# Performance work log

Measured on AMD Instinct MI355X. Metric: run time of the kernel, lower is better.

## Reference

```python
import jax, jax.numpy as jnp
import numpy as np

N = 50000; E = 800000
GNN_IN = 256; MLP_IN = 256; HID = 512; F_DIM = 128; H = 2; NCLS = 40
HC = H * F_DIM  # 256


def setup_inputs() -> dict:
    key = jax.random.key(0)
    ks = jax.random.split(key, 24)
    w = lambda k, shape: (jax.random.normal(k, shape, jnp.float32) * 0.05)
    inp = {
        'x_gsage': jax.random.normal(ks[0], (N, GNN_IN), jnp.float32),
        'edge_index': jax.random.randint(ks[1], (2, E), 0, N),
        'x_mlp': jax.random.normal(ks[2], (N, MLP_IN), jnp.float32),
        # TransformerConv params (query/key/value/skip linears)
        'Wq': w(ks[3], (HC, GNN_IN)), 'bq': jnp.zeros(HC, jnp.float32),
        'Wk': w(ks[4], (HC, GNN_IN)), 'bk': jnp.zeros(HC, jnp.float32),
        'Wv': w(ks[5], (HC, GNN_IN)), 'bv': jnp.zeros(HC, jnp.float32),
        'Wskip': w(ks[6], (HC, GNN_IN)), 'bskip': jnp.zeros(HC, jnp.float32),
        # MLP (num_layers=3): in->hid, hid->hid, hid->2*F_DIM; 2 batchnorms
        'W1': w(ks[7], (HID, MLP_IN)), 'b1': jnp.zeros(HID, jnp.float32),
        'g1': jnp.ones(HID, jnp.float32), 'be1': jnp.zeros(HID, jnp.float32),
        'W2': w(ks[8], (HID, HID)), 'b2': jnp.zeros(HID, jnp.float32),
        'g2': jnp.ones(HID, jnp.float32), 'be2': jnp.zeros(HID, jnp.float32),
        'W3': w(ks[9], (HC, HID)), 'b3': jnp.zeros(HC, jnp.float32),
        # fusion scalars
        'alpha': jnp.array([0.5], jnp.float32), 'beta': jnp.array([0.5], jnp.float32),
        # classifier head
        'Wc1': w(ks[10], (HID, HC)), 'bc1': jnp.zeros(HID, jnp.float32),
        'Wc2': w(ks[11], (NCLS, HID)), 'bc2': jnp.zeros(NCLS, jnp.float32),
    }
    return inp


def _lin(x, W, b):
    return x @ W.T + b


def _batchnorm(x, g, b, eps=1e-5):
    mu = jnp.mean(x, axis=0)
    var = jnp.var(x, axis=0)
    return (x - mu) * jax.lax.rsqrt(var + eps) * g + b


def _transformer_conv(x, edge_index, Wq, bq, Wk, bk, Wv, bv, Wskip, bskip):
    # PyG TransformerConv, heads=H, concat=True, root_weight=True (eval: no dropout)
    q = _lin(x, Wq, bq).reshape(N, H, F_DIM)
    k = _lin(x, Wk, bk).reshape(N, H, F_DIM)
    v = _lin(x, Wv, bv).reshape(N, H, F_DIM)
    src, dst = edge_index[0], edge_index[1]
    # per-edge, per-head attention logits  [E, H]
    logits = jnp.einsum('ehd,ehd->eh', q[dst], k[src]) / jnp.sqrt(jnp.float32(F_DIM))
    # segment softmax over incoming edges of each destination node
    amax = jax.ops.segment_max(logits, dst, num_segments=N)  # [N, H]
    amax = jnp.where(jnp.isfinite(amax), amax, 0.0)
    ex = jnp.exp(logits - amax[dst])                           # [E, H]
    denom = jax.ops.segment_sum(ex, dst, num_segments=N)      # [N, H]
    attn = ex / jnp.maximum(denom[dst], 1e-16)                 # [E, H]
    msg = v[src] * attn[:, :, None]                            # [E, H, C]
    out = jax.ops.segment_sum(msg, dst, num_segments=N)       # [N, H, C]
    out = out.reshape(N, HC) + _lin(x, Wskip, bskip)
    return out


def reference(x_gsage, edge_index, x_mlp, Wq, bq, Wk, bk, Wv, bv, Wskip, bskip,
              W1, b1, g1, be1, W2, b2, g2, be2, W3, b3, alpha, beta,
              Wc1, bc1, Wc2, bc2):
    h_g = _transformer_conv(x_gsage, edge_index, Wq, bq, Wk, bk, Wv, bv, Wskip, bskip)
    # MLP branch: (lin -> BN(batch stats) -> sigmoid) x2, then final lin; dropout off (eval)
    h = jax.nn.sigmoid(_batchnorm(_lin(x_mlp, W1, b1), g1, be1))
    h = jax.nn.sigmoid(_batchnorm(_lin(h, W2, b2), g2, be2))
    h_m = _lin(h, W3, b3)
    h_fused = alpha * h_g + beta * h_m
    out = _lin(jax.nn.relu(_lin(h_fused, Wc1, bc1)), Wc2, bc2)
    return out
```

## Files before the change

### kernel.cpp

```cpp
#include <hip/hip_runtime.h>
#include <hip/hip_bf16.h>
#include <cstdint>
#include <cstddef>

typedef __attribute__((ext_vector_type(8))) short short8;
typedef __attribute__((ext_vector_type(4))) float f32x4;

__device__ inline ushort f2bs(float f) {
    __hip_bfloat16 h = __float2bfloat16(f);
    return *(ushort*)&h;
}
__device__ inline float bu2f(ushort u) {
    return __uint_as_float(((unsigned)u) << 16);
}

template <int AB, int BM, int KT, int SIG>
__global__ __launch_bounds__(256) void gemm_fullk(
    const void* __restrict__ Avoid, const short* __restrict__ Wb,
    const float* __restrict__ bias, ushort* __restrict__ C,
    const float* __restrict__ scale, const float* __restrict__ shift,
    int M, int NT, int act)
{
    constexpr int KQ = KT / 32;
    __shared__ short As[BM][KT + 8];
    __shared__ short Bs[128][40];

    const int tid = threadIdx.x;
    const int lane = tid & 63;
    const int w = tid >> 6;
    const int wm = w >> 1, wn = w & 1;
    constexpr int MI = BM / 32;
    const int m0 = blockIdx.x * BM;
    const int lr = lane & 15;
    const int lk = (lane >> 4) * 8;
    const int Ntot = NT * 128;

    {
        constexpr int TPR = KT / 128;
        const int arow = tid / TPR;
        const int ac0 = (tid % TPR) * 128;
        const bool ok = (m0 + arow) < M;
        if (AB == 0) {
            const float* ap = (const float*)Avoid + (size_t)(m0 + arow) * KT + ac0;
#pragma unroll
            for (int j = 0; j < 16; ++j) {
                float4 x = ok ? *(const float4*)(ap + j * 8)
                              : make_float4(0.f, 0.f, 0.f, 0.f);
                float4 y = ok ? *(const float4*)(ap + j * 8 + 4)
                              : make_float4(0.f, 0.f, 0.f, 0.f);
                short8 v;
                v[0] = f2bs(x.x); v[1] = f2bs(x.y); v[2] = f2bs(x.z); v[3] = f2bs(x.w);
                v[4] = f2bs(y.x); v[5] = f2bs(y.y); v[6] = f2bs(y.z); v[7] = f2bs(y.w);
                *(short8*)&As[arow][ac0 + j * 8] = v;
            }
        } else {
            const short* ap = (const short*)Avoid + (size_t)(m0 + arow) * KT + ac0;
#pragma unroll
            for (int j = 0; j < 16; ++j) {
                short8 v = {};
                if (ok) v = *(const short8*)(ap + j * 8);
                if (SIG) {
#pragma unroll
                    for (int e = 0; e < 8; ++e) {
                        int c = ac0 + j * 8 + e;
                        float f = bu2f((ushort)v[e]) * scale[c] + shift[c];
                        v[e] = (short)f2bs(1.f / (1.f + __expf(-f)));
                    }
                }
                *(short8*)&As[arow][ac0 + j * 8] = v;
            }
        }
    }

    const int trow = tid >> 1;
    const int tcg = (tid & 1) * 16;

    short8 r0, r1;
    {
        const short* wp = Wb + (size_t)trow * KT + tcg;
        r0 = *(const short8*)wp;
        r1 = *(const short8*)(wp + 8);
    }

    f32x4 acc[MI][4] = {};
    const int total = NT * KQ;

    for (int idx = 0; idx < total; ++idx) {
        *(short8*)&Bs[trow][tcg] = r0;
        *(short8*)&Bs[trow][tcg + 8] = r1;
        __syncthreads();

        const int nidx = idx + 1;
        if (nidx < total) {
            const int nt = nidx / KQ, nk = (nidx % KQ) * 32;
            const short* wp = Wb + (size_t)(nt * 128 + trow) * KT + nk + tcg;
            r0 = *(const short8*)wp;
            r1 = *(const short8*)(wp + 8);
        }

        const int k0 = (idx % KQ) * 32;
        short8 afr[MI], bfr[4];
#pragma unroll
        for (int mi = 0; mi < MI; ++mi)
            afr[mi] = *(const short8*)&As[wm * (BM / 2) + mi * 16 + lr][k0 + lk];
#pragma unroll
        for (int nj = 0; nj < 4; ++nj)
            bfr[nj] = *(const short8*)&Bs[wn * 64 + nj * 16 + lr][lk];
#pragma unroll
        for (int mi = 0; mi < MI; ++mi)
#pragma unroll
            for (int nj = 0; nj < 4; ++nj)
                acc[mi][nj] = __builtin_amdgcn_mfma_f32_16x16x32_bf16(
                    afr[mi], bfr[nj], acc[mi][nj], 0, 0, 0);
        __syncthreads();

        if ((idx % KQ) == KQ - 1) {
            const int t = idx / KQ;
#pragma unroll
            for (int mi = 0; mi < MI; ++mi) {
#pragma unroll
                for (int nj = 0; nj < 4; ++nj) {
                    int gn = t * 128 + wn * 64 + nj * 16 + lr;
                    float b = bias[gn];
#pragma unroll
                    for (int r = 0; r < 4; ++r) {
                        int gm = m0 + wm * (BM / 2) + mi * 16 + (lane >> 4) * 4 + r;
                        if (gm < M) {
                            float v = acc[mi][nj][r] + b;
                            if (act == 1) v = fmaxf(v, 0.f);
                            C[(size_t)gm * Ntot + gn] = f2bs(v);
                        }
                    }
                    acc[mi][nj] = (f32x4){0.f, 0.f, 0.f, 0.f};
                }
            }
        }
    }
}

__global__ __launch_bounds__(256) void mfma_gemm_small(
    const short* __restrict__ A, const float* __restrict__ W,
    const float* __restrict__ bias, float* __restrict__ Cf,
    int M, int K, int Nout)
{
    __shared__ short As[128][40];
    __shared__ short Bs[128][40];
    const int tid = threadIdx.x;
    const int lane = tid & 63;
    const int w = tid >> 6;
    const int wm = w >> 1, wn = w & 1;
    const int m0 = blockIdx.y * 128, n0 = blockIdx.x * 128;
    const int trow = tid >> 1;
    const int tcg = (tid & 1) * 16;
    const int lr = lane & 15;
    const int lk = (lane >> 4) * 8;

    f32x4 acc[4][4] = {};

    for (int k0 = 0; k0 < K; k0 += 32) {
        {
            bool ok = (m0 + trow) < M;
            const short* ap = A + (size_t)(m0 + trow) * K + k0 + tcg;
            short8 s0 = {}, s1 = {};
            if (ok) { s0 = *(const short8*)(ap); s1 = *(const short8*)(ap + 8); }
            *(short8*)&As[trow][tcg] = s0;
            *(short8*)&As[trow][tcg + 8] = s1;
        }
        {
            short v[16];
            bool ok = (n0 + trow) < Nout;
            const float* wp = W + (size_t)(n0 + trow) * K + k0 + tcg;
#pragma unroll
            for (int q = 0; q < 4; ++q) {
                float4 t4 = ok ? *(const float4*)(wp + q * 4)
                               : make_float4(0.f, 0.f, 0.f, 0.f);
                v[q * 4 + 0] = f2bs(t4.x); v[q * 4 + 1] = f2bs(t4.y);
                v[q * 4 + 2] = f2bs(t4.z); v[q * 4 + 3] = f2bs(t4.w);
            }
            short8 w0, w1;
#pragma unroll
            for (int j = 0; j < 8; ++j) { w0[j] = v[j]; w1[j] = v[j + 8]; }
            *(short8*)&Bs[trow][tcg] = w0;
            *(short8*)&Bs[trow][tcg + 8] = w1;
        }
        __syncthreads();
        short8 afr[4], bfr[4];
#pragma unroll
        for (int mi = 0; mi < 4; ++mi)
            afr[mi] = *(const short8*)&As[wm * 64 + mi * 16 + lr][lk];
#pragma unroll
        for (int nj = 0; nj < 4; ++nj)
            bfr[nj] = *(const short8*)&Bs[wn * 64 + nj * 16 + lr][lk];
#pragma unroll
        for (int mi = 0; mi < 4; ++mi)
#pragma unroll
            for (int nj = 0; nj < 4; ++nj)
                acc[mi][nj] = __builtin_amdgcn_mfma_f32_16x16x32_bf16(
                    afr[mi], bfr[nj], acc[mi][nj], 0, 0, 0);
        __syncthreads();
    }
#pragma unroll
    for (int mi = 0; mi < 4; ++mi)
#pragma unroll
        for (int nj = 0; nj < 4; ++nj) {
            int gn = n0 + wn * 64 + nj * 16 + lr;
            if (gn >= Nout) continue;
            float b = bias[gn];
#pragma unroll
            for (int r = 0; r < 4; ++r) {
                int gm = m0 + wm * 64 + mi * 16 + (lane >> 4) * 4 + r;
                if (gm < M) Cf[(size_t)gm * Nout + gn] = acc[mi][nj][r] + b;
            }
        }
}

__global__ void zero_words(unsigned* __restrict__ p, size_t n)
{
    size_t i = (size_t)blockIdx.x * blockDim.x + threadIdx.x;
    size_t stride = (size_t)gridDim.x * blockDim.x;
    for (; i < n; i += stride) p[i] = 0u;
}

__global__ void pack_params(
    const float* __restrict__ Wq, const float* __restrict__ Wk,
    const float* __restrict__ Wv, const float* __restrict__ Wskip,
    const float* __restrict__ W1, const float* __restrict__ W2,
    const float* __restrict__ W3, const float* __restrict__ Wc1,
    const float* __restrict__ bq, const float* __restrict__ bk,
    const float* __restrict__ bv, const float* __restrict__ bskip,
    ushort* __restrict__ Wall, float* __restrict__ bcat)
{
    int q = blockIdx.x * 256 + threadIdx.x;
    if (q < 229376) {
        const float* s; int base4;
        if      (q < 16384)  { s = Wq;    base4 = 0; }
        else if (q < 32768)  { s = Wk;    base4 = 16384; }
        else if (q < 49152)  { s = Wv;    base4 = 32768; }
        else if (q < 65536)  { s = Wskip; base4 = 49152; }
        else if (q < 98304)  { s = W1;    base4 = 65536; }
        else if (q < 163840) { s = W2;    base4 = 98304; }
        else if (q < 196608) { s = W3;    base4 = 163840; }
        else                 { s = Wc1;   base4 = 196608; }
        float4 v = ((const float4*)s)[q - base4];
        ushort4 o;
        o.x = f2bs(v.x); o.y = f2bs(v.y); o.z = f2bs(v.z); o.w = f2bs(v.w);
        ((ushort4*)Wall)[q] = o;
    } else if (q < 229632) {
        int j = q - 229376;
        const float* s = (j < 64) ? bq : (j < 128) ? bk : (j < 192) ? bv : bskip;
        ((float4*)bcat)[j] = ((const float4*)s)[j & 63];
    }
}

__global__ __launch_bounds__(256) void bn_stats512_b(
    const ushort* __restrict__ X, float* __restrict__ sums,
    float* __restrict__ sumsq, int M)
{
    int t = threadIdx.x;
    float s0 = 0.f, q0 = 0.f, s1 = 0.f, q1 = 0.f;
    for (int r = blockIdx.x; r < M; r += gridDim.x) {
        ushort2 v = *(const ushort2*)(X + (size_t)r * 512 + 2 * t);
        float a = bu2f(v.x), b = bu2f(v.y);
        s0 += a; q0 += a * a;
        s1 += b; q1 += b * b;
    }
    atomicAdd(&sums[2 * t], s0);
    atomicAdd(&sumsq[2 * t], q0);
    atomicAdd(&sums[2 * t + 1], s1);
    atomicAdd(&sumsq[2 * t + 1], q1);
}

__global__ void bn_finalize(const float* __restrict__ sums,
                            const float* __restrict__ sumsq,
                            const float* __restrict__ g,
                            const float* __restrict__ be,
                            float* __restrict__ scale, float* __restrict__ shift,
                            int M, int C)
{
    int c = blockIdx.x * blockDim.x + threadIdx.x;
    if (c >= C) return;
    float mean = sums[c] / (float)M;
    float var = sumsq[c] / (float)M - mean * mean;
    float inv = rsqrtf(var + 1e-5f);
    float sc = g[c] * inv;
    scale[c] = sc;
    shift[c] = be[c] - mean * sc;
}

__global__ void count_edges(const int* __restrict__ ei, int* __restrict__ counts, int E)
{
    int i = blockIdx.x * 256 + threadIdx.x;
    if (i < E) atomicAdd(&counts[ei[E + i]], 1);
}

__global__ __launch_bounds__(256) void scan_local(
    const int* __restrict__ cnt, int* __restrict__ excl,
    int* __restrict__ bsums, int n)
{
    __shared__ int s[256];
    int t = threadIdx.x;
    int i = blockIdx.x * 256 + t;
    int v = (i < n) ? cnt[i] : 0;
    s[t] = v;
    __syncthreads();
    for (int off = 1; off < 256; off <<= 1) {
        int u = (t >= off) ? s[t - off] : 0;
        __syncthreads();
        s[t] += u;
        __syncthreads();
    }
    if (i < n) excl[i] = s[t] - v;
    if (t == 255) bsums[blockIdx.x] = s[255];
}

__global__ __launch_bounds__(256) void scan_top(int* __restrict__ bsums, int nb)
{
    __shared__ int s[256];
    int t = threadIdx.x;
    int v = (t < nb) ? bsums[t] : 0;
    s[t] = v;
    __syncthreads();
    for (int off = 1; off < 256; off <<= 1) {
        int u = (t >= off) ? s[t - off] : 0;
        __syncthreads();
        s[t] += u;
        __syncthreads();
    }
    if (t < nb) bsums[t] = s[t] - v;
}

__global__ void scan_add(int* __restrict__ excl, const int* __restrict__ bsums,
                         int* __restrict__ cursor, int n)
{
    int i = blockIdx.x * 256 + threadIdx.x;
    if (i < n) {
        int v = excl[i] + bsums[blockIdx.x];
        excl[i] = v;
        cursor[i] = v;
    }
}

__global__ void fill_edges(const int* __restrict__ ei, int* __restrict__ cursor,
                           int* __restrict__ esrc, int E)
{
    int i = blockIdx.x * 256 + threadIdx.x;
    if (i < E) {
        int dst = ei[E + i];
        int pos = atomicAdd(&cursor[dst], 1);
        esrc[pos] = ei[i];
    }
}

__global__ __launch_bounds__(256) void edge_attn(
    const int* __restrict__ esrc, const int* __restrict__ offs,
    const int* __restrict__ cnts, const ushort* __restrict__ QKVS,
    const ushort* __restrict__ hmb, const float* __restrict__ alpha,
    const float* __restrict__ beta, ushort* __restrict__ hf, int N)
{
    int node = blockIdx.x * 4 + (threadIdx.x >> 6);
    int lane = threadIdx.x & 63;
    if (node >= N) return;
    int start = offs[node];
    int cnt = cnts[node];

    ushort4 qu = *(const ushort4*)(QKVS + (size_t)node * 1024 + lane * 4);
    float qx = bu2f(qu.x), qy = bu2f(qu.y), qz = bu2f(qu.z), qw = bu2f(qu.w);
    const float s = 0.088388347648318447f;

    float m = -INFINITY, d = 0.f;
    float a0 = 0.f, a1 = 0.f, a2 = 0.f, a3 = 0.f;

    ushort4 ku_n = {}, vu_n = {};
    if (cnt > 0) {
        int src0 = esrc[start];
        ku_n = *(const ushort4*)(QKVS + (size_t)src0 * 1024 + 256 + lane * 4);
        vu_n = *(const ushort4*)(QKVS + (size_t)src0 * 1024 + 512 + lane * 4);
    }
    for (int i = 0; i < cnt; ++i) {
        ushort4 ku = ku_n, vu = vu_n;
        if (i + 1 < cnt) {
            int srcn = esrc[start + i + 1];
            ku_n = *(const ushort4*)(QKVS + (size_t)srcn * 1024 + 256 + lane * 4);
            vu_n = *(const ushort4*)(QKVS + (size_t)srcn * 1024 + 512 + lane * 4);
        }
        float p = qx * bu2f(ku.x) + qy * bu2f(ku.y)
                + qz * bu2f(ku.z) + qw * bu2f(ku.w);
        p += __shfl_xor(p, 1);
        p += __shfl_xor(p, 2);
        p += __shfl_xor(p, 4);
        p += __shfl_xor(p, 8);
        p += __shfl_xor(p, 16);
        float l = p * s;
        float mn = fmaxf(m, l);
        float sc = __expf(m - mn);
        float pe = __expf(l - mn);
        d = d * sc + pe;
        a0 = a0 * sc + pe * bu2f(vu.x);
        a1 = a1 * sc + pe * bu2f(vu.y);
        a2 = a2 * sc + pe * bu2f(vu.z);
        a3 = a3 * sc + pe * bu2f(vu.w);
        m = mn;
    }
    float invd = (cnt > 0) ? 1.f / fmaxf(d, 1e-16f) : 0.f;
    float o0 = a0 * invd, o1 = a1 * invd, o2 = a2 * invd, o3 = a3 * invd;

    ushort4 su = *(const ushort4*)(QKVS + (size_t)node * 1024 + 768 + lane * 4);
    ushort4 hm = *(const ushort4*)(hmb + (size_t)node * 256 + lane * 4);
    float al = alpha[0], be = beta[0];
    ushort4 o;
    o.x = f2bs(al * (o0 + bu2f(su.x)) + be * bu2f(hm.x));
    o.y = f2bs(al * (o1 + bu2f(su.y)) + be * bu2f(hm.y));
    o.z = f2bs(al * (o2 + bu2f(su.z)) + be * bu2f(hm.z));
    o.w = f2bs(al * (o3 + bu2f(su.w)) + be * bu2f(hm.w));
    *(ushort4*)(hf + (size_t)node * 256 + lane * 4) = o;
}

extern "C" void kernel_launch(void* const* d_in, const int* in_sizes, int n_in,
                              void* d_out, int out_size, void* d_ws, size_t ws_size,
                              hipStream_t stream)
{
    const float* x_g   = (const float*)d_in[0];
    const int*   ei    = (const int*)d_in[1];
    const float* x_m   = (const float*)d_in[2];
    const float* Wq    = (const float*)d_in[3];
    const float* bq    = (const float*)d_in[4];
    const float* Wk    = (const float*)d_in[5];
    const float* bk    = (const float*)d_in[6];
    const float* Wv    = (const float*)d_in[7];
    const float* bv    = (const float*)d_in[8];
    const float* Wskip = (const float*)d_in[9];
    const float* bskip = (const float*)d_in[10];
    const float* W1    = (const float*)d_in[11];
    const float* b1    = (const float*)d_in[12];
    const float* g1    = (const float*)d_in[13];
    const float* be1   = (const float*)d_in[14];
    const float* W2    = (const float*)d_in[15];
    const float* b2    = (const float*)d_in[16];
    const float* g2    = (const float*)d_in[17];
    const float* be2   = (const float*)d_in[18];
    const float* W3    = (const float*)d_in[19];
    const float* b3    = (const float*)d_in[20];
    const float* alpha = (const float*)d_in[21];
    const float* beta  = (const float*)d_in[22];
    const float* Wc1   = (const float*)d_in[23];
    const float* bc1   = (const float*)d_in[24];
    const float* Wc2   = (const float*)d_in[25];
    const float* bc2   = (const float*)d_in[26];
    float* out = (float*)d_out;

    const int N = in_sizes[0] / 256;
    const int E = in_sizes[1] / 2;

    float* ws = (float*)d_ws;
    ushort* QKVS = (ushort*)ws;
    ushort* bufA = (ushort*)(ws + (size_t)N * 512);
    ushort* bufB = (ushort*)(ws + (size_t)N * 768);
    ushort* hmb  = (ushort*)(ws + (size_t)N * 1024);
    float* wz = ws + (size_t)N * 1152;

    float* sum1 = wz, *sq1 = wz + 512, *sum2 = wz + 1024, *sq2 = wz + 1536;
    int* counts = (int*)(wz + 2048);
    float* wz2 = wz + 2048 + N;
    float* scale1 = wz2, *shift1 = wz2 + 512;
    float* scale2 = wz2 + 1024, *shift2 = wz2 + 1536;
    int* bsums = (int*)(wz2 + 2048);
    int* offs = bsums + 256;
    int* cursor = offs + N;
    int* esrc = cursor + N;
    short* Wall = (short*)(esrc + E);
    float* bcat = (float*)(Wall + 917504);
    const short* Wcat = Wall;
    const short* W1b  = Wall + 262144;
    const short* W2b  = Wall + 393216;
    const short* W3b  = Wall + 655360;
    const short* Wc1b = Wall + 786432;

    dim3 blk(256);

    hipLaunchKernelGGL(zero_words, dim3(128), blk, 0, stream,
                       (unsigned*)wz, (size_t)(2048 + N));

    hipLaunchKernelGGL(pack_params, dim3(898), blk, 0, stream,
                       Wq, Wk, Wv, Wskip, W1, W2, W3, Wc1,
                       bq, bk, bv, bskip, (ushort*)Wall, bcat);

    const int nb = (N + 255) / 256;
    hipLaunchKernelGGL(count_edges, dim3((E + 255) / 256), blk, 0, stream, ei, counts, E);
    hipLaunchKernelGGL(scan_local, dim3(nb), blk, 0, stream, counts, offs, bsums, N);
    hipLaunchKernelGGL(scan_top, dim3(1), blk, 0, stream, bsums, nb);
    hipLaunchKernelGGL(scan_add, dim3(nb), blk, 0, stream, offs, bsums, cursor, N);
    hipLaunchKernelGGL(fill_edges, dim3((E + 255) / 256), blk, 0, stream, ei, cursor, esrc, E);

    const int g128 = (N + 127) / 128;
    const int g64 = (N + 63) / 64;

    hipLaunchKernelGGL((gemm_fullk<0, 128, 256, 0>), dim3(g128), blk, 0, stream,
                       x_m, W1b, b1, bufA, nullptr, nullptr, N, 4, 0);
    hipLaunchKernelGGL(bn_stats512_b, dim3(512), blk, 0, stream, bufA, sum1, sq1, N);
    hipLaunchKernelGGL(bn_finalize, dim3(2), blk, 0, stream, sum1, sq1, g1, be1, scale1, shift1, N, 512);
    hipLaunchKernelGGL((gemm_fullk<1, 64, 512, 1>), dim3(g64), blk, 0, stream,
                       bufA, W2b, b2, bufB, scale1, shift1, N, 4, 0);
    hipLaunchKernelGGL(bn_stats512_b, dim3(512), blk, 0, stream, bufB, sum2, sq2, N);
    hipLaunchKernelGGL(bn_finalize, dim3(2), blk, 0, stream, sum2, sq2, g2, be2, scale2, shift2, N, 512);
    hipLaunchKernelGGL((gemm_fullk<1, 64, 512, 1>), dim3(g64), blk, 0, stream,
                       bufB, W3b, b3, hmb, scale2, shift2, N, 2, 0);

    hipLaunchKernelGGL((gemm_fullk<0, 128, 256, 0>), dim3(g128), blk, 0, stream,
                       x_g, Wcat, bcat, QKVS, nullptr, nullptr, N, 8, 0);

    hipLaunchKernelGGL(edge_attn, dim3((N + 3) / 4), blk, 0, stream,
                       esrc, offs, counts, QKVS, hmb, alpha, beta, bufA, N);

    hipLaunchKernelGGL((gemm_fullk<1, 128, 256, 0>), dim3(g128), blk, 0, stream,
                       bufA, Wc1b, bc1, bufB, nullptr, nullptr, N, 4, 1);
    hipLaunchKernelGGL(mfma_gemm_small, dim3(1, (N + 127) / 128), blk, 0, stream,
                       (const short*)bufB, Wc2, bc2, out, N, 512, 40);
}
```

Before: 962.6 us.

## Swizzle GEMM shared memory, widen K step, merge QKVS and MLP1 launches

Rewrites the full-K GEMM so the A and B shared tiles use an XOR swizzle instead of padding, which targets LDS bank conflicts. The K step per iteration grows from 32 to 64, halving the number of barrier pairs per output tile. The QKVS projection and the first MLP linear now run in one launch that picks its operands by block index, so two independent GEMMs share a grid and one launch is removed. Shared memory use changes and the B prefetch uses more registers, which may lower occupancy.

```diff
diff --git a/kernel.cpp b/kernel.cpp
--- a/kernel.cpp
+++ b/kernel.cpp
@@ -15,33 +15,51 @@
 }
 
 template <int AB, int BM, int KT, int SIG>
-__global__ __launch_bounds__(256) void gemm_fullk(
-    const void* __restrict__ Avoid, const short* __restrict__ Wb,
-    const float* __restrict__ bias, ushort* __restrict__ C,
-    const float* __restrict__ scale, const float* __restrict__ shift,
-    int M, int NT, int act)
-{
-    constexpr int KQ = KT / 32;
-    __shared__ short As[BM][KT + 8];
-    __shared__ short Bs[128][40];
+__global__ __launch_bounds__(256) void gemm_v2(
+    const void* __restrict__ A0, const short* __restrict__ W0,
+    const float* __restrict__ bias0, ushort* __restrict__ C0, int NT0,
+    const void* __restrict__ A1, const short* __restrict__ W1,
+    const float* __restrict__ bias1, ushort* __restrict__ C1, int NT1,
+    int split, const float* __restrict__ scale, const float* __restrict__ shift,
+    int M, int act)
+{
+    constexpr int KQ = KT / 64;
+    constexpr int MI = BM / 32;
+    __shared__ short As[BM * KT];
+    __shared__ short Bs[128 * 64];
 
     const int tid = threadIdx.x;
     const int lane = tid & 63;
     const int w = tid >> 6;
     const int wm = w >> 1, wn = w & 1;
-    constexpr int MI = BM / 32;
-    const int m0 = blockIdx.x * BM;
     const int lr = lane & 15;
-    const int lk = (lane >> 4) * 8;
+    const int lkc = lane >> 4;
+
+    const int bsel = (blockIdx.x < (unsigned)split) ? 0 : 1;
+    const void* Av = bsel ? A1 : A0;
+    const short* Wb = bsel ? W1 : W0;
+    const float* bias = bsel ? bias1 : bias0;
+    ushort* C = bsel ? C1 : C0;
+    const int NT = bsel ? NT1 : NT0;
+    const int bx = bsel ? ((int)blockIdx.x - split) : (int)blockIdx.x;
+    const int m0 = bx * BM;
     const int Ntot = NT * 128;
+
+    const int btr = tid >> 1;
+    const int bc0 = (tid & 1) * 4;
+    short8 pb[4];
+#pragma unroll
+    for (int j = 0; j < 4; ++j)
+        pb[j] = *(const short8*)(Wb + (size_t)btr * KT + (bc0 + j) * 8);
 
     {
         constexpr int TPR = KT / 128;
-        const int arow = tid / TPR;
-        const int ac0 = (tid % TPR) * 128;
-        const bool ok = (m0 + arow) < M;
+        const int ar = tid / TPR;
+        const int cg0 = (tid % TPR) * 16;
+        const bool ok = (m0 + ar) < M;
+        const int sw = ar & 7;
         if (AB == 0) {
-            const float* ap = (const float*)Avoid + (size_t)(m0 + arow) * KT + ac0;
+            const float* ap = (const float*)Av + (size_t)(m0 + ar) * KT + cg0 * 8;
 #pragma unroll
             for (int j = 0; j < 16; ++j) {
                 float4 x = ok ? *(const float4*)(ap + j * 8)
@@ -51,10 +69,10 @@
                 short8 v;
                 v[0] = f2bs(x.x); v[1] = f2bs(x.y); v[2] = f2bs(x.z); v[3] = f2bs(x.w);
                 v[4] = f2bs(y.x); v[5] = f2bs(y.y); v[6] = f2bs(y.z); v[7] = f2bs(y.w);
-                *(short8*)&As[arow][ac0 + j * 8] = v;
+                *(short8*)&As[ar * KT + ((cg0 + j) ^ sw) * 8] = v;
             }
         } else {
-            const short* ap = (const short*)Avoid + (size_t)(m0 + arow) * KT + ac0;
+            const short* ap = (const short*)Av + (size_t)(m0 + ar) * KT + cg0 * 8;
 #pragma unroll
             for (int j = 0; j < 16; ++j) {
                 short8 v = {};
@@ -62,56 +80,61 @@
                 if (SIG) {
 #pragma unroll
                     for (int e = 0; e < 8; ++e) {
-                        int c = ac0 + j * 8 + e;
+                        int c = (cg0 + j) * 8 + e;
                         float f = bu2f((ushort)v[e]) * scale[c] + shift[c];
                         v[e] = (short)f2bs(1.f / (1.f + __expf(-f)));
                     }
                 }
-                *(short8*)&As[arow][ac0 + j * 8] = v;
-            }
-        }
-    }
-
-    const int trow = tid >> 1;
-    const int tcg = (tid & 1) * 16;
-
-    short8 r0, r1;
-    {
-        const short* wp = Wb + (size_t)trow * KT + tcg;
-        r0 = *(const short8*)wp;
-        r1 = *(const short8*)(wp + 8);
+                *(short8*)&As[ar * KT + ((cg0 + j) ^ sw) * 8] = v;
+            }
+        }
     }
 
     f32x4 acc[MI][4] = {};
     const int total = NT * KQ;
+    const int bsw = btr & 7;
 
     for (int idx = 0; idx < total; ++idx) {
-        *(short8*)&Bs[trow][tcg] = r0;
-        *(short8*)&Bs[trow][tcg + 8] = r1;
+#pragma unroll
+        for (int j = 0; j < 4; ++j)
+            *(short8*)&Bs[btr * 64 + ((bc0 + j) ^ bsw) * 8] = pb[j];
         __syncthreads();
 
         const int nidx = idx + 1;
         if (nidx < total) {
-            const int nt = nidx / KQ, nk = (nidx % KQ) * 32;
-            const short* wp = Wb + (size_t)(nt * 128 + trow) * KT + nk + tcg;
-            r0 = *(const short8*)wp;
-            r1 = *(const short8*)(wp + 8);
-        }
-
-        const int k0 = (idx % KQ) * 32;
-        short8 afr[MI], bfr[4];
-#pragma unroll
-        for (int mi = 0; mi < MI; ++mi)
-            afr[mi] = *(const short8*)&As[wm * (BM / 2) + mi * 16 + lr][k0 + lk];
-#pragma unroll
-        for (int nj = 0; nj < 4; ++nj)
-            bfr[nj] = *(const short8*)&Bs[wn * 64 + nj * 16 + lr][lk];
-#pragma unroll
-        for (int mi = 0; mi < MI; ++mi)
-#pragma unroll
-            for (int nj = 0; nj < 4; ++nj)
-                acc[mi][nj] = __builtin_amdgcn_mfma_f32_16x16x32_bf16(
-                    afr[mi], bfr[nj], acc[mi][nj], 0, 0, 0);
+            const int nt = nidx / KQ, nk = (nidx % KQ) * 64;
+            const short* wp = Wb + (size_t)(nt * 128 + btr) * KT + nk + bc0 * 8;
+#pragma unroll
+            for (int j = 0; j < 4; ++j)
+                pb[j] = *(const short8*)(wp + j * 8);
+        }
+
+        const int kc = (idx % KQ) * 8;
+        short8 afr[2][MI], bfr[2][4];
+#pragma unroll
+        for (int s = 0; s < 2; ++s)
+#pragma unroll
+            for (int mi = 0; mi < MI; ++mi) {
+                int r = wm * (BM / 2) + mi * 16 + lr;
+                int cg = kc + s * 4 + lkc;
+                afr[s][mi] = *(const short8*)&As[r * KT + (cg ^ (r & 7)) * 8];
+            }
+#pragma unroll
+        for (int s = 0; s < 2; ++s)
+#pragma unroll
+            for (int nj = 0; nj < 4; ++nj) {
+                int r = wn * 64 + nj * 16 + lr;
+                int cg = s * 4 + lkc;
+                bfr[s][nj] = *(const short8*)&Bs[r * 64 + (cg ^ (r & 7)) * 8];
+            }
+#pragma unroll
+        for (int s = 0; s < 2; ++s)
+#pragma unroll
+            for (int mi = 0; mi < MI; ++mi)
+#pragma unroll
+                for (int nj = 0; nj < 4; ++nj)
+                    acc[mi][nj] = __builtin_amdgcn_mfma_f32_16x16x32_bf16(
+                        afr[s][mi], bfr[s][nj], acc[mi][nj], 0, 0, 0);
         __syncthreads();
 
         if ((idx % KQ) == KQ - 1) {
@@ -494,25 +517,31 @@
     const int g128 = (N + 127) / 128;
     const int g64 = (N + 63) / 64;
 
-    hipLaunchKernelGGL((gemm_fullk<0, 128, 256, 0>), dim3(g128), blk, 0, stream,
-                       x_m, W1b, b1, bufA, nullptr, nullptr, N, 4, 0);
+    hipLaunchKernelGGL((gemm_v2<0, 128, 256, 0>), dim3(2 * g128), blk, 0, stream,
+                       x_g, Wcat, bcat, QKVS, 8,
+                       x_m, W1b, b1, bufA, 4,
+                       g128, nullptr, nullptr, N, 0);
+
     hipLaunchKernelGGL(bn_stats512_b, dim3(512), blk, 0, stream, bufA, sum1, sq1, N);
     hipLaunchKernelGGL(bn_finalize, dim3(2), blk, 0, stream, sum1, sq1, g1, be1, scale1, shift1, N, 512);
-    hipLaunchKernelGGL((gemm_fullk<1, 64, 512, 1>), dim3(g64), blk, 0, stream,
-                       bufA, W2b, b2, bufB, scale1, shift1, N, 4, 0);
+    hipLaunchKernelGGL((gemm_v2<1, 64, 512, 1>), dim3(g64), blk, 0, stream,
+                       bufA, W2b, b2, bufB, 4,
+                       bufA, W2b, b2, bufB, 4,
+                       2 * g64, scale1, shift1, N, 0);
     hipLaunchKernelGGL(bn_stats512_b, dim3(512), blk, 0, stream, bufB, sum2, sq2, N);
     hipLaunchKernelGGL(bn_finalize, dim3(2), blk, 0, stream, sum2, sq2, g2, be2, scale2, shift2, N, 512);
-    hipLaunchKernelGGL((gemm_fullk<1, 64, 512, 1>), dim3(g64), blk, 0, stream,
-                       bufB, W3b, b3, hmb, scale2, shift2, N, 2, 0);
-
-    hipLaunchKernelGGL((gemm_fullk<0, 128, 256, 0>), dim3(g128), blk, 0, stream,
-                       x_g, Wcat, bcat, QKVS, nullptr, nullptr, N, 8, 0);
+    hipLaunchKernelGGL((gemm_v2<1, 64, 512, 1>), dim3(g64), blk, 0, stream,
+                       bufB, W3b, b3, hmb, 2,
+                       bufB, W3b, b3, hmb, 2,
+                       2 * g64, scale2, shift2, N, 0);
 
     hipLaunchKernelGGL(edge_attn, dim3((N + 3) / 4), blk, 0, stream,
                        esrc, offs, counts, QKVS, hmb, alpha, beta, bufA, N);
 
-    hipLaunchKernelGGL((gemm_fullk<1, 128, 256, 0>), dim3(g128), blk, 0, stream,
-                       bufA, Wc1b, bc1, bufB, nullptr, nullptr, N, 4, 1);
+    hipLaunchKernelGGL((gemm_v2<1, 128, 256, 0>), dim3(g128), blk, 0, stream,
+                       bufA, Wc1b, bc1, bufB, 4,
+                       bufA, Wc1b, bc1, bufB, 4,
+                       2 * g128, nullptr, nullptr, N, 1);
     hipLaunchKernelGGL(mfma_gemm_small, dim3(1, (N + 127) / 128), blk, 0, stream,
                        (const short*)bufB, Wc2, bc2, out, N, 512, 40);
 }
```

New measurement: 929.0 us. 3.5% less time.
